# Performance work log

Measured on AMD Instinct MI355X. Metric: run time of the kernel, lower is better.

Reference implementation:

```python
import jax, jax.numpy as jnp
import numpy as np

B, S, D = 8, 2048, 1024
E, K = 16, 2
H = 4096
SD, SH = D // E, H // E  # 64, 256
MAX_SEQ = 2048


def setup_inputs() -> dict:
    key = jax.random.key(0)
    ks = jax.random.split(key, 5)
    x = jax.random.normal(ks[0], (B, S, D), dtype=jnp.float32)
    w_switch = jax.random.normal(ks[1], (D * MAX_SEQ, E), dtype=jnp.float32) * 0.001
    b_switch = jnp.zeros((E,), dtype=jnp.float32)
    w1 = jax.random.normal(ks[2], (E, SD, SH), dtype=jnp.float32) * (1.0 / np.sqrt(SD))
    b1 = jnp.zeros((E, SH), dtype=jnp.float32)
    w2 = jax.random.normal(ks[3], (H, D), dtype=jnp.float32) * (1.0 / np.sqrt(H))
    b2 = jnp.zeros((D,), dtype=jnp.float32)
    return {"x": x, "w_switch": w_switch, "b_switch": b_switch,
            "w1": w1, "b1": b1, "w2": w2, "b2": b2}


def reference(x, w_switch, b_switch, w1, b1, w2, b2):
    # Router: softmax over experts from flattened first MAX_SEQ tokens
    x0 = x[:, :MAX_SEQ].reshape(B, -1)                      # [B, D*MAX_SEQ]
    route_prob = jax.nn.softmax(x0 @ w_switch + b_switch)   # [B, E]
    # Top-k expert membership mask per batch element
    _, topk_idx = jax.lax.top_k(route_prob, K)              # [B, K]
    mask = jax.nn.one_hot(topk_idx, E, dtype=x.dtype).sum(axis=1)  # [B, E]
    # Per-expert linear on the expert's channel slice, masked combine
    xe = x.reshape(B, S, E, SD)                              # [B, S, E, SD]
    h = jnp.einsum('bsed,edh->bseh', xe, w1) + b1            # [B, S, E, SH]
    h = h * mask[:, None, :, None]                           # zero out non-routed
    out = h.reshape(B, S, H)                                 # [B, S, H]
    out = jax.nn.gelu(out, approximate=False)                # exact GELU (torch default)
    return out @ w2 + b2                                     # [B, S, D]
```

## Files before the change

kernel.cpp:

```cpp
#include <hip/hip_runtime.h>
#include <hip/hip_bf16.h>

#define B_  8
#define S_  2048
#define D_  1024
#define E_  16
#define SD_ 64
#define SH_ 256
#define H_  4096
#define R_  (D_ * S_)
#define NBLK_ 8192
#define NCVT_ 2176

typedef __attribute__((ext_vector_type(8))) short bf16x8;
typedef __attribute__((ext_vector_type(4))) float f32x4;

static __device__ __forceinline__ short f2bf(float f) {
    union { float f; unsigned u; } v; v.f = f;
    unsigned r = v.u + 0x7fffu + ((v.u >> 16) & 1u);
    return (short)(r >> 16);
}

__global__ __launch_bounds__(256, 4) void router_conv_kernel(
        const float* __restrict__ x, const float* __restrict__ wsw,
        const float* __restrict__ w1, const float* __restrict__ w2,
        float* __restrict__ partials, short* __restrict__ w1f,
        short* __restrict__ w2f) {
    if (blockIdx.x >= NBLK_) {
        int blk = blockIdx.x - NBLK_;
        if (blk < 128) {
            int t = blk * 256 + threadIdx.x;
            int lane = t & 63, ntile = (t >> 6) & 15, ks = (t >> 10) & 1, e = t >> 11;
            int k0 = ks * 32 + ((lane >> 4) << 3);
            int n  = (ntile << 4) + (lane & 15);
            const float* src = w1 + ((size_t)(e * 64 + k0) * 256 + n);
            bf16x8 o;
            #pragma unroll
            for (int j = 0; j < 8; ++j) o[j] = f2bf(src[(size_t)j * 256]);
            *(bf16x8*)(w1f + ((size_t)t << 3)) = o;
        } else {
            int t = (blk - 128) * 256 + threadIdx.x;
            int lane = t & 63, ntile = (t >> 6) & 63, kg = t >> 12;
            int k0 = (kg << 5) + ((lane >> 4) << 3);
            int n  = (ntile << 4) + (lane & 15);
            const float* src = w2 + ((size_t)k0 * 1024 + n);
            bf16x8 o;
            #pragma unroll
            for (int j = 0; j < 8; ++j) o[j] = f2bf(src[(size_t)j * 1024]);
            *(bf16x8*)(w2f + ((size_t)t << 3)) = o;
        }
        return;
    }

    __shared__ float red[512];
    int tid = threadIdx.x;
    int wid = tid >> 6, lane = tid & 63;
    int q = lane & 3, rsub = lane >> 2;
    size_t wavebase = (((size_t)blockIdx.x << 2) + wid) << 6;
    const f32x4* wp = (const f32x4*)wsw + (wavebase << 2) + lane;

    f32x4 w0 = wp[0];
    f32x4 w1v = wp[64];
    f32x4 w2v = wp[128];
    f32x4 w3v = wp[192];
    float xv[4][8];
    #pragma unroll
    for (int b = 0; b < 8; ++b) {
        const float* xb = x + (size_t)b * R_ + wavebase + rsub;
        #pragma unroll
        for (int it = 0; it < 4; ++it)
            xv[it][b] = xb[it << 4];
    }

    float acc[8][4];
    #pragma unroll
    for (int b = 0; b < 8; ++b)
        #pragma unroll
        for (int j = 0; j < 4; ++j) acc[b][j] = 0.f;

    #define FMA4(W, IT)                                             \
        _Pragma("unroll")                                           \
        for (int b = 0; b < 8; ++b) {                               \
            float xs = xv[IT][b];                                   \
            acc[b][0] = fmaf(xs, (W)[0], acc[b][0]);                \
            acc[b][1] = fmaf(xs, (W)[1], acc[b][1]);                \
            acc[b][2] = fmaf(xs, (W)[2], acc[b][2]);                \
            acc[b][3] = fmaf(xs, (W)[3], acc[b][3]);                \
        }
    FMA4(w0, 0)
    FMA4(w1v, 1)
    FMA4(w2v, 2)
    FMA4(w3v, 3)
    #undef FMA4

    #pragma unroll
    for (int b = 0; b < 8; ++b)
        #pragma unroll
        for (int j = 0; j < 4; ++j) {
            float v = acc[b][j];
            v += __shfl_xor(v, 4);
            v += __shfl_xor(v, 8);
            v += __shfl_xor(v, 16);
            v += __shfl_xor(v, 32);
            acc[b][j] = v;
        }

    if (lane < 4) {
        #pragma unroll
        for (int b = 0; b < 8; ++b)
            #pragma unroll
            for (int j = 0; j < 4; ++j)
                red[(wid << 7) + b * 16 + q * 4 + j] = acc[b][j];
    }
    __syncthreads();
    if (tid < 128)
        partials[(size_t)blockIdx.x * 128 + tid] =
            red[tid] + red[128 + tid] + red[256 + tid] + red[384 + tid];
}

__global__ __launch_bounds__(256) void reduce_kernel(const float* __restrict__ partials,
                                                     float* __restrict__ part2) {
    __shared__ float sred[4][128];
    int j = blockIdx.x, tid = threadIdx.x;
    int col4 = tid & 31, rg = tid >> 5;
    const f32x4* p4 = (const f32x4*)partials;

    f32x4 acc = (f32x4){0.f, 0.f, 0.f, 0.f};
    #pragma unroll
    for (int p = 0; p < 8; ++p) {
        f32x4 v = p4[(size_t)(j * 64 + p * 8 + rg) * 32 + col4];
        acc[0] += v[0]; acc[1] += v[1]; acc[2] += v[2]; acc[3] += v[3];
    }
    #pragma unroll
    for (int k = 0; k < 4; ++k) acc[k] += __shfl_xor(acc[k], 32);

    int wid = tid >> 6, lane = tid & 63;
    if (lane < 32) {
        #pragma unroll
        for (int k = 0; k < 4; ++k) sred[wid][lane * 4 + k] = acc[k];
    }
    __syncthreads();
    if (tid < 128)
        part2[(size_t)j * 128 + tid] =
            sred[0][tid] + sred[1][tid] + sred[2][tid] + sred[3][tid];
}

__global__ __launch_bounds__(128) void topk_kernel(const float* __restrict__ part2,
                                                   const float* __restrict__ bsw,
                                                   int* __restrict__ experts) {
    __shared__ float vlog[128];
    int tid = threadIdx.x;
    float t = 0.f;
    #pragma unroll 8
    for (int j = 0; j < 128; ++j) t += part2[(size_t)j * 128 + tid];
    vlog[tid] = t + bsw[tid & 15];
    __syncthreads();
    if (tid < 8) {
        float v[16];
        #pragma unroll
        for (int e = 0; e < 16; ++e) v[e] = vlog[tid * 16 + e];
        int i0 = 0; float m0 = v[0];
        #pragma unroll
        for (int e = 1; e < 16; ++e) if (v[e] > m0) { m0 = v[e]; i0 = e; }
        int i1 = -1; float m1 = -3.4e38f;
        #pragma unroll
        for (int e = 0; e < 16; ++e) if (e != i0 && v[e] > m1) { m1 = v[e]; i1 = e; }
        experts[2 * tid]     = i0;
        experts[2 * tid + 1] = i1;
    }
}

__global__ __launch_bounds__(512, 4) void mlp_kernel(
        const float* __restrict__ x, const int* __restrict__ experts,
        const short* __restrict__ w1f, const float* __restrict__ b1,
        const short* __restrict__ w2f, const float* __restrict__ b2,
        float* __restrict__ out) {
    __shared__ short G[32][520];

    int blk  = blockIdx.x;
    int b    = blk & 7;
    int tok0 = (blk >> 3) << 5;
    int e0 = experts[2 * b], e1 = experts[2 * b + 1];
    int tid = threadIdx.x;
    int wid = tid >> 6, lane = tid & 63;
    int lrow = lane & 15, lk8 = (lane >> 4) << 3;
    int r0 = (lane >> 4) << 2;

    {
        int slot  = wid >> 2;
        int ex    = slot ? e1 : e0;
        int nhalf = (wid >> 1) & 1;
        int mh    = wid & 1;

        f32x4 acc1[8];
        #pragma unroll
        for (int n = 0; n < 8; ++n) acc1[n] = (f32x4){0.f, 0.f, 0.f, 0.f};

        #pragma unroll
        for (int ks = 0; ks < 2; ++ks) {
            const float* xp = x + (((size_t)b * S_ + tok0 + mh * 16 + lrow) * D_
                                   + ex * 64 + ks * 32 + lk8);
            float4 f0 = *(const float4*)xp;
            float4 f1 = *(const float4*)(xp + 4);
            bf16x8 a;
            a[0] = f2bf(f0.x); a[1] = f2bf(f0.y); a[2] = f2bf(f0.z); a[3] = f2bf(f0.w);
            a[4] = f2bf(f1.x); a[5] = f2bf(f1.y); a[6] = f2bf(f1.z); a[7] = f2bf(f1.w);
            #pragma unroll
            for (int nt = 0; nt < 8; ++nt) {
                int ntg = nhalf * 8 + nt;
                bf16x8 bf = *(const bf16x8*)(w1f + ((((size_t)(ex * 2 + ks) * 16 + ntg) * 64 + lane) << 3));
                acc1[nt] = __builtin_amdgcn_mfma_f32_16x16x32_bf16(a, bf, acc1[nt], 0, 0, 0);
            }
        }

        #pragma unroll
        for (int nt = 0; nt < 8; ++nt) {
            int ncol = (nhalf * 8 + nt) * 16 + lrow;
            float bb = b1[ex * 256 + ncol];
            #pragma unroll
            for (int r = 0; r < 4; ++r) {
                float v = acc1[nt][r] + bb;
                v = 0.5f * v * (1.0f + erff(v * 0.70710678118f));
                G[mh * 16 + r0 + r][slot * 256 + ncol] = f2bf(v);
            }
        }
    }
    __syncthreads();

    f32x4 acc2[2][8];
    #pragma unroll
    for (int m = 0; m < 2; ++m)
        #pragma unroll
        for (int n = 0; n < 8; ++n) acc2[m][n] = (f32x4){0.f, 0.f, 0.f, 0.f};

    for (int ks = 0; ks < 16; ++ks) {
        int e  = (ks < 8) ? e0 : e1;
        int kg = e * 8 + (ks & 7);
        bf16x8 a0 = *(const bf16x8*)&G[lrow][ks * 32 + lk8];
        bf16x8 a1 = *(const bf16x8*)&G[16 + lrow][ks * 32 + lk8];
        #pragma unroll
        for (int nt = 0; nt < 8; ++nt) {
            int ntg = wid * 8 + nt;
            bf16x8 bf = *(const bf16x8*)(w2f + ((((size_t)kg * 64 + ntg) * 64 + lane) << 3));
            acc2[0][nt] = __builtin_amdgcn_mfma_f32_16x16x32_bf16(a0, bf, acc2[0][nt], 0, 0, 0);
            acc2[1][nt] = __builtin_amdgcn_mfma_f32_16x16x32_bf16(a1, bf, acc2[1][nt], 0, 0, 0);
        }
    }

    size_t obase = ((size_t)b * S_ + tok0) * D_;
    #pragma unroll
    for (int nt = 0; nt < 8; ++nt) {
        int d = wid * 128 + nt * 16 + lrow;
        float bb = b2[d];
        #pragma unroll
        for (int m = 0; m < 2; ++m) {
            int rr = m * 16 + r0;
            #pragma unroll
            for (int r = 0; r < 4; ++r)
                out[obase + (size_t)(rr + r) * D_ + d] = acc2[m][nt][r] + bb;
        }
    }
}

extern "C" void kernel_launch(void* const* d_in, const int* in_sizes, int n_in,
                              void* d_out, int out_size, void* d_ws, size_t ws_size,
                              hipStream_t stream) {
    const float* x   = (const float*)d_in[0];
    const float* wsw = (const float*)d_in[1];
    const float* bsw = (const float*)d_in[2];
    const float* w1  = (const float*)d_in[3];
    const float* b1  = (const float*)d_in[4];
    const float* w2  = (const float*)d_in[5];
    const float* b2  = (const float*)d_in[6];
    float* out = (float*)d_out;

    int*   experts  = (int*)d_ws;
    float* partials = (float*)((char*)d_ws + 4096);
    float* part2    = (float*)((char*)d_ws + 4096 + 4194304);
    short* w1f = (short*)((char*)d_ws + 4096 + 4194304 + 65536);
    short* w2f = (short*)((char*)d_ws + 4096 + 4194304 + 65536 + 524288);

    router_conv_kernel<<<NBLK_ + NCVT_, 256, 0, stream>>>(x, wsw, w1, w2,
                                                          partials, w1f, w2f);
    reduce_kernel<<<128, 256, 0, stream>>>(partials, part2);
    topk_kernel<<<1, 128, 0, stream>>>(part2, bsw, experts);
    mlp_kernel<<<512, 512, 0, stream>>>(x, experts, w1f, b1, w2f, b2, out);
}
```

Measured before the change: 110.4 us.

## Fold top-k into MLP kernel via atomic logits and enlarge MLP tile to 64 tokens

Removes the single-block topk kernel. The reduce kernel now atomically accumulates logits into a buffer zeroed in the first kernel, and each MLP block computes its own top-2 experts from those logits. The MLP kernel also grows to 1024 threads handling 64 tokens per block, with 4x4 MFMA tiles per wave, so each w2 fragment is reused across more rows. This saves a launch and a serialized step, at the cost of float atomics (non-deterministic summation order) and fewer, larger blocks (256).

```diff
diff --git a/kernel.cpp b/kernel.cpp
--- a/kernel.cpp
+++ b/kernel.cpp
@@ -25,9 +25,10 @@
         const float* __restrict__ x, const float* __restrict__ wsw,
         const float* __restrict__ w1, const float* __restrict__ w2,
         float* __restrict__ partials, short* __restrict__ w1f,
-        short* __restrict__ w2f) {
+        short* __restrict__ w2f, float* __restrict__ logits) {
     if (blockIdx.x >= NBLK_) {
         int blk = blockIdx.x - NBLK_;
+        if (blk == 0 && threadIdx.x < 128) logits[threadIdx.x] = 0.f;
         if (blk < 128) {
             int t = blk * 256 + threadIdx.x;
             int lane = t & 63, ntile = (t >> 6) & 15, ks = (t >> 10) & 1, e = t >> 11;
@@ -119,7 +120,7 @@
 }
 
 __global__ __launch_bounds__(256) void reduce_kernel(const float* __restrict__ partials,
-                                                     float* __restrict__ part2) {
+                                                     float* __restrict__ logits) {
     __shared__ float sred[4][128];
     int j = blockIdx.x, tid = threadIdx.x;
     int col4 = tid & 31, rg = tid >> 5;
@@ -141,56 +142,47 @@
     }
     __syncthreads();
     if (tid < 128)
-        part2[(size_t)j * 128 + tid] =
-            sred[0][tid] + sred[1][tid] + sred[2][tid] + sred[3][tid];
-}
-
-__global__ __launch_bounds__(128) void topk_kernel(const float* __restrict__ part2,
-                                                   const float* __restrict__ bsw,
-                                                   int* __restrict__ experts) {
-    __shared__ float vlog[128];
-    int tid = threadIdx.x;
-    float t = 0.f;
-    #pragma unroll 8
-    for (int j = 0; j < 128; ++j) t += part2[(size_t)j * 128 + tid];
-    vlog[tid] = t + bsw[tid & 15];
-    __syncthreads();
-    if (tid < 8) {
-        float v[16];
-        #pragma unroll
-        for (int e = 0; e < 16; ++e) v[e] = vlog[tid * 16 + e];
-        int i0 = 0; float m0 = v[0];
-        #pragma unroll
-        for (int e = 1; e < 16; ++e) if (v[e] > m0) { m0 = v[e]; i0 = e; }
-        int i1 = -1; float m1 = -3.4e38f;
-        #pragma unroll
-        for (int e = 0; e < 16; ++e) if (e != i0 && v[e] > m1) { m1 = v[e]; i1 = e; }
-        experts[2 * tid]     = i0;
-        experts[2 * tid + 1] = i1;
-    }
-}
-
-__global__ __launch_bounds__(512, 4) void mlp_kernel(
-        const float* __restrict__ x, const int* __restrict__ experts,
+        atomicAdd(&logits[tid],
+                  sred[0][tid] + sred[1][tid] + sred[2][tid] + sred[3][tid]);
+}
+
+__global__ __launch_bounds__(1024, 4) void mlp_kernel(
+        const float* __restrict__ x, const float* __restrict__ logits,
+        const float* __restrict__ bsw,
         const short* __restrict__ w1f, const float* __restrict__ b1,
         const short* __restrict__ w2f, const float* __restrict__ b2,
         float* __restrict__ out) {
-    __shared__ short G[32][520];
+    __shared__ short G[64][520];
+    __shared__ float vlog[16];
+    __shared__ int se[2];
 
     int blk  = blockIdx.x;
     int b    = blk & 7;
-    int tok0 = (blk >> 3) << 5;
-    int e0 = experts[2 * b], e1 = experts[2 * b + 1];
+    int tok0 = (blk >> 3) << 6;
     int tid = threadIdx.x;
     int wid = tid >> 6, lane = tid & 63;
     int lrow = lane & 15, lk8 = (lane >> 4) << 3;
     int r0 = (lane >> 4) << 2;
 
+    if (tid < 16) vlog[tid] = logits[b * 16 + tid] + bsw[tid];
+    __syncthreads();
+    if (tid == 0) {
+        int i0 = 0; float m0 = vlog[0];
+        #pragma unroll
+        for (int e = 1; e < 16; ++e) if (vlog[e] > m0) { m0 = vlog[e]; i0 = e; }
+        int i1 = -1; float m1 = -3.4e38f;
+        #pragma unroll
+        for (int e = 0; e < 16; ++e) if (e != i0 && vlog[e] > m1) { m1 = vlog[e]; i1 = e; }
+        se[0] = i0; se[1] = i1;
+    }
+    __syncthreads();
+    int e0 = se[0], e1 = se[1];
+
     {
-        int slot  = wid >> 2;
+        int slot  = wid >> 3;
         int ex    = slot ? e1 : e0;
-        int nhalf = (wid >> 1) & 1;
-        int mh    = wid & 1;
+        int nhalf = (wid >> 2) & 1;
+        int mq    = wid & 3;
 
         f32x4 acc1[8];
         #pragma unroll
@@ -198,7 +190,7 @@
 
         #pragma unroll
         for (int ks = 0; ks < 2; ++ks) {
-            const float* xp = x + (((size_t)b * S_ + tok0 + mh * 16 + lrow) * D_
+            const float* xp = x + (((size_t)b * S_ + tok0 + mq * 16 + lrow) * D_
                                    + ex * 64 + ks * 32 + lk8);
             float4 f0 = *(const float4*)xp;
             float4 f1 = *(const float4*)(xp + 4);
@@ -221,39 +213,43 @@
             for (int r = 0; r < 4; ++r) {
                 float v = acc1[nt][r] + bb;
                 v = 0.5f * v * (1.0f + erff(v * 0.70710678118f));
-                G[mh * 16 + r0 + r][slot * 256 + ncol] = f2bf(v);
+                G[mq * 16 + r0 + r][slot * 256 + ncol] = f2bf(v);
             }
         }
     }
     __syncthreads();
 
-    f32x4 acc2[2][8];
-    #pragma unroll
-    for (int m = 0; m < 2; ++m)
-        #pragma unroll
-        for (int n = 0; n < 8; ++n) acc2[m][n] = (f32x4){0.f, 0.f, 0.f, 0.f};
+    f32x4 acc2[4][4];
+    #pragma unroll
+    for (int m = 0; m < 4; ++m)
+        #pragma unroll
+        for (int n = 0; n < 4; ++n) acc2[m][n] = (f32x4){0.f, 0.f, 0.f, 0.f};
 
     for (int ks = 0; ks < 16; ++ks) {
         int e  = (ks < 8) ? e0 : e1;
         int kg = e * 8 + (ks & 7);
         bf16x8 a0 = *(const bf16x8*)&G[lrow][ks * 32 + lk8];
         bf16x8 a1 = *(const bf16x8*)&G[16 + lrow][ks * 32 + lk8];
-        #pragma unroll
-        for (int nt = 0; nt < 8; ++nt) {
-            int ntg = wid * 8 + nt;
+        bf16x8 a2 = *(const bf16x8*)&G[32 + lrow][ks * 32 + lk8];
+        bf16x8 a3 = *(const bf16x8*)&G[48 + lrow][ks * 32 + lk8];
+        #pragma unroll
+        for (int nt = 0; nt < 4; ++nt) {
+            int ntg = wid * 4 + nt;
             bf16x8 bf = *(const bf16x8*)(w2f + ((((size_t)kg * 64 + ntg) * 64 + lane) << 3));
             acc2[0][nt] = __builtin_amdgcn_mfma_f32_16x16x32_bf16(a0, bf, acc2[0][nt], 0, 0, 0);
             acc2[1][nt] = __builtin_amdgcn_mfma_f32_16x16x32_bf16(a1, bf, acc2[1][nt], 0, 0, 0);
+            acc2[2][nt] = __builtin_amdgcn_mfma_f32_16x16x32_bf16(a2, bf, acc2[2][nt], 0, 0, 0);
+            acc2[3][nt] = __builtin_amdgcn_mfma_f32_16x16x32_bf16(a3, bf, acc2[3][nt], 0, 0, 0);
         }
     }
 
     size_t obase = ((size_t)b * S_ + tok0) * D_;
     #pragma unroll
-    for (int nt = 0; nt < 8; ++nt) {
-        int d = wid * 128 + nt * 16 + lrow;
+    for (int nt = 0; nt < 4; ++nt) {
+        int d = wid * 64 + nt * 16 + lrow;
         float bb = b2[d];
         #pragma unroll
-        for (int m = 0; m < 2; ++m) {
+        for (int m = 0; m < 4; ++m) {
             int rr = m * 16 + r0;
             #pragma unroll
             for (int r = 0; r < 4; ++r)
@@ -274,15 +270,13 @@
     const float* b2  = (const float*)d_in[6];
     float* out = (float*)d_out;
 
-    int*   experts  = (int*)d_ws;
+    float* logits   = (float*)d_ws;
     float* partials = (float*)((char*)d_ws + 4096);
-    float* part2    = (float*)((char*)d_ws + 4096 + 4194304);
-    short* w1f = (short*)((char*)d_ws + 4096 + 4194304 + 65536);
-    short* w2f = (short*)((char*)d_ws + 4096 + 4194304 + 65536 + 524288);
+    short* w1f = (short*)((char*)d_ws + 4096 + 4194304);
+    short* w2f = (short*)((char*)d_ws + 4096 + 4194304 + 524288);
 
     router_conv_kernel<<<NBLK_ + NCVT_, 256, 0, stream>>>(x, wsw, w1, w2,
-                                                          partials, w1f, w2f);
-    reduce_kernel<<<128, 256, 0, stream>>>(partials, part2);
-    topk_kernel<<<1, 128, 0, stream>>>(part2, bsw, experts);
-    mlp_kernel<<<512, 512, 0, stream>>>(x, experts, w1f, b1, w2f, b2, out);
-}
+                                                          partials, w1f, w2f, logits);
+    reduce_kernel<<<128, 256, 0, stream>>>(partials, logits);
+    mlp_kernel<<<256, 1024, 0, stream>>>(x, logits, bsw, w1f, b1, w2f, b2, out);
+}
```

After: 111.2 us. About the same (+0.8%).
